# Kernel tuning notes

Hardware: AMD Instinct MI355X
Metric: run time of the kernel (lower is better)

Reference implementation:

```python
import jax, jax.numpy as jnp
import numpy as np

B, L, D, T = 32, 512, 1024, 256
MAX_MENTION_LEN = 10
NEG_INF = float('-inf')


def _static_bounds_and_keep():
    # Full (start, end) grid, flattened row-major like torch's .view(-1, 2)
    s = np.repeat(np.arange(L), L)
    e = np.tile(np.arange(L), L)
    bounds = np.stack([s, e], axis=-1)            # [L*L, 2]
    keep = (e - s) <= MAX_MENTION_LEN             # static per-position mask
    idx = np.nonzero(keep)[0]
    return jnp.asarray(bounds[keep], jnp.int32), jnp.asarray(idx, jnp.int32)


def setup_inputs() -> dict:
    key = jax.random.key(0)
    k0, k1, k2 = jax.random.split(key, 3)
    text_encodings = jax.random.normal(k0, (B, L, D), dtype=jnp.float32)
    mask_ctxt = jnp.ones((B, L), dtype=jnp.int32)
    # word -> wordpiece mapping: [start, end_exclusive); values kept in [1, L)
    tokens_mapping = jax.random.randint(k1, (B, T, 2), 1, L).astype(jnp.int32)
    W = jax.random.normal(k2, (D, 3), dtype=jnp.float32) * 0.02
    b = jnp.zeros((3,), dtype=jnp.float32)
    return {"text_encodings": text_encodings, "mask_ctxt": mask_ctxt,
            "tokens_mapping": tokens_mapping, "W": W, "b": b}


def reference(text_encodings, mask_ctxt, tokens_mapping, W, b):
    # per-token start / end / mention logits
    logits = jnp.einsum('bld,dk->blk', text_encodings, W) + b  # [B, L, 3]
    valid_tok = (mask_ctxt == 1)
    start_lp = jnp.where(valid_tok, logits[:, :, 0], NEG_INF)
    end_lp = jnp.where(valid_tok, logits[:, :, 1], NEG_INF)
    mention_lp = jnp.where(valid_tok, logits[:, :, 2], NEG_INF)

    # scores[b, s, e] = start[b, s] + end[b, e] + sum_{i=s..e} mention[b, i]
    scores = start_lp[:, :, None] + end_lp[:, None, :]          # [B, L, L]
    csum = jnp.cumsum(mention_lp, axis=1)                        # [B, L]
    csum_prev = jnp.concatenate(
        [jnp.zeros((csum.shape[0], 1), csum.dtype), csum[:, :-1]], axis=1)
    scores = scores + (csum[:, None, :] - csum_prev[:, :, None])

    # mention_sizes > 0  <=>  e >= s
    pos = jnp.arange(L)
    size_ok = pos[None, :, None] <= pos[None, None, :]           # [1, L, L]

    # token-boundary masks (scatter 1 at word starts / ends, zero col 0)
    bidx = jnp.arange(tokens_mapping.shape[0])[:, None]
    ts = jnp.zeros(mask_ctxt.shape, jnp.int32).at[bidx, tokens_mapping[:, :, 0]].set(1)
    ts = ts.at[:, 0].set(0)
    te = jnp.zeros(mask_ctxt.shape, jnp.int32).at[bidx, tokens_mapping[:, :, 1] - 1].set(1)
    te = te.at[:, 0].set(0)
    vse = ts[:, :, None] * te[:, None, :]                        # bmm outer product

    valid = size_ok & (mask_ctxt[:, :, None] > 0) & (vse > 0)
    scores = jnp.where(valid, scores, NEG_INF)

    scores_flat = scores.reshape(scores.shape[0], -1)            # [B, L*L]
    bounds_keep, keep_idx = _static_bounds_and_keep()
    out_scores = scores_flat[:, keep_idx]                        # [B, K]
    out_bounds = jnp.broadcast_to(bounds_keep[None],
                                  (scores.shape[0],) + bounds_keep.shape)
    return out_scores, out_bounds
```

## Files before the change

### kernel.cpp

```cpp
#include <hip/hip_runtime.h>
#include <math.h>

#define BB 32
#define LL 512
#define DD 1024
#define TT 256
#define NK 136393
#define NK_LIN 131273
#define S_LIN 502
#define NEG_BIG  -3.0e38f
#define NEG_MASK -1.0e30f

typedef float f4v __attribute__((ext_vector_type(4)));
typedef float f2v __attribute__((ext_vector_type(2)));

__global__ __launch_bounds__(256) void logits_kernel(
    const float* __restrict__ text, const float* __restrict__ W,
    const float* __restrict__ bias, const int* __restrict__ mask,
    const int* __restrict__ tmap,
    float* __restrict__ slp, float* __restrict__ elp, float* __restrict__ mlp,
    int* __restrict__ fs, int* __restrict__ fe)
{
    __shared__ int tsl[LL];
    __shared__ int tel[LL];
    const int wid  = threadIdx.x >> 6;
    const int lane = threadIdx.x & 63;
    const int row  = blockIdx.x * 4 + wid;
    const int b    = blockIdx.x;
    const int t    = threadIdx.x;

    if (b < BB) {
        tsl[t] = 0; tsl[t + 256] = 0;
        tel[t] = 0; tel[t + 256] = 0;
        __syncthreads();
        int s0 = tmap[((size_t)b * TT + t) * 2 + 0];
        int e0 = tmap[((size_t)b * TT + t) * 2 + 1] - 1;
        s0 = min(max(s0, 0), LL - 1);
        e0 = min(max(e0, 0), LL - 1);
        tsl[s0] = 1;
        tel[e0] = 1;
        __syncthreads();
    }

    const f4v* t4 = (const f4v*)(text + (size_t)row * DD);
    const f4v* w4 = (const f4v*)W;
    float a0 = 0.f, a1 = 0.f, a2 = 0.f;
#pragma unroll
    for (int j = 0; j < 4; ++j) {
        const int fi = lane + j * 64;
        f4v v  = __builtin_nontemporal_load(&t4[fi]);
        f4v w0 = w4[fi * 3 + 0];
        f4v w1 = w4[fi * 3 + 1];
        f4v w2 = w4[fi * 3 + 2];
        a0 += v.x * w0.x;  a1 += v.x * w0.y;  a2 += v.x * w0.z;
        a0 += v.y * w0.w;  a1 += v.y * w1.x;  a2 += v.y * w1.y;
        a0 += v.z * w1.z;  a1 += v.z * w1.w;  a2 += v.z * w2.x;
        a0 += v.w * w2.y;  a1 += v.w * w2.z;  a2 += v.w * w2.w;
    }
#pragma unroll
    for (int off = 32; off; off >>= 1) {
        a0 += __shfl_down(a0, off);
        a1 += __shfl_down(a1, off);
        a2 += __shfl_down(a2, off);
    }
    if (lane == 0) {
        const int m = mask[row];
        slp[row] = (m == 1) ? a0 + bias[0] : NEG_MASK;
        elp[row] = (m == 1) ? a1 + bias[1] : NEG_MASK;
        mlp[row] = (m == 1) ? a2 + bias[2] : NEG_MASK;
    }

    if (b < BB) {
        const int i0 = b * LL + t, i1 = i0 + 256;
        fs[i0] = (t != 0 && mask[i0] == 1 && tsl[t]) ? 1 : 0;
        fs[i1] = (mask[i1] == 1 && tsl[t + 256]) ? 1 : 0;
        fe[i0] = (t != 0 && tel[t]) ? 1 : 0;
        fe[i1] = tel[t + 256] ? 1 : 0;
    }
}

__global__ __launch_bounds__(256) void out_kernel(
    const float* __restrict__ slp, const float* __restrict__ elp,
    const float* __restrict__ mlp,
    const int* __restrict__ fs, const int* __restrict__ fe,
    float* __restrict__ out)
{
    const int s = blockIdx.x;
    const int b = blockIdx.y;
    const int t = threadIdx.x;
    const int rowlen = min(LL, s + 11);
    const size_t obase = (size_t)b * NK +
        (s <= S_LIN ? s * (s + 21) / 2 : NK_LIN + (s - S_LIN) * LL);
    const int base = b * LL;
    const int   fss = fs[base + s];
    const float sv  = slp[base + s];
    f2v* bptr = (f2v*)(out + (size_t)BB * NK);

#pragma unroll
    for (int h = 0; h < 2; ++h) {
        const int e = t + h * 256;
        if (e < rowlen) {
            float score = NEG_BIG;
            if (e >= s && fss && fe[base + e]) {
                float w = 0.f;
                for (int l = s; l <= e; ++l) w += mlp[base + l];
                score = (sv + elp[base + e]) + w;
            }
            __builtin_nontemporal_store(score, &out[obase + e]);
            f2v bv; bv.x = (float)s; bv.y = (float)e;
            __builtin_nontemporal_store(bv, &bptr[obase + e]);
        }
    }
}

extern "C" void kernel_launch(void* const* d_in, const int* in_sizes, int n_in,
                              void* d_out, int out_size, void* d_ws, size_t ws_size,
                              hipStream_t stream) {
    const float* text = (const float*)d_in[0];
    const int*   mask = (const int*)d_in[1];
    const int*   tmap = (const int*)d_in[2];
    const float* W    = (const float*)d_in[3];
    const float* bias = (const float*)d_in[4];
    float* out = (float*)d_out;

    float* slp = (float*)d_ws;
    float* elp = slp + (size_t)BB * LL;
    float* mlp = elp + (size_t)BB * LL;
    int*   fs  = (int*)(mlp + (size_t)BB * LL);
    int*   fe  = fs + (size_t)BB * LL;

    logits_kernel<<<BB * LL / 4, 256, 0, stream>>>(text, W, bias, mask, tmap,
                                                   slp, elp, mlp, fs, fe);
    dim3 g2(LL, BB);
    out_kernel<<<g2, 256, 0, stream>>>(slp, elp, mlp, fs, fe, out);
}
```

Measured before the change: 32.34 us.

## Fuse logits and output kernels into one block-per-row-range kernel

Merges the logits projection and the span-score writer into one kernel. Each block handles one batch and one of 16 row ranges, computing logits for its rows plus a 10-row halo into shared memory and then writing scores and bounds. The ranges come from a fixed split table chosen to balance output sizes, and the block-to-batch mapping groups each batch's blocks onto one XCD. This removes a launch and the workspace round trip, at the cost of recomputing halo rows and having only 512 blocks to hide latency.

```diff
diff --git a/kernel.cpp b/kernel.cpp
--- a/kernel.cpp
+++ b/kernel.cpp
@@ -10,105 +10,107 @@
 #define S_LIN 502
 #define NEG_BIG  -3.0e38f
 #define NEG_MASK -1.0e30f
+#define NRANGE 16
+#define MAXROWS 64
 
 typedef float f4v __attribute__((ext_vector_type(4)));
 typedef float f2v __attribute__((ext_vector_type(2)));
 
-__global__ __launch_bounds__(256) void logits_kernel(
+__device__ __constant__ int d_splits[NRANGE + 1] =
+    {0, 51, 97, 138, 177, 212, 246, 277, 308, 336, 364, 391, 417, 441, 466, 489, 512};
+
+__device__ __forceinline__ int off_s(int s) {
+    return (s <= S_LIN) ? s * (s + 21) / 2 : NK_LIN + (s - S_LIN) * LL;
+}
+
+__global__ __launch_bounds__(512, 4) void fused_kernel(
     const float* __restrict__ text, const float* __restrict__ W,
     const float* __restrict__ bias, const int* __restrict__ mask,
-    const int* __restrict__ tmap,
-    float* __restrict__ slp, float* __restrict__ elp, float* __restrict__ mlp,
-    int* __restrict__ fs, int* __restrict__ fe)
+    const int* __restrict__ tmap, float* __restrict__ out)
 {
-    __shared__ int tsl[LL];
-    __shared__ int tel[LL];
-    const int wid  = threadIdx.x >> 6;
-    const int lane = threadIdx.x & 63;
-    const int row  = blockIdx.x * 4 + wid;
-    const int b    = blockIdx.x;
-    const int t    = threadIdx.x;
+    __shared__ float sl[MAXROWS], el[MAXROWS], ml[MAXROWS];
+    __shared__ unsigned char tsl[LL], tel[LL];
 
-    if (b < BB) {
-        tsl[t] = 0; tsl[t + 256] = 0;
-        tel[t] = 0; tel[t + 256] = 0;
-        __syncthreads();
-        int s0 = tmap[((size_t)b * TT + t) * 2 + 0];
-        int e0 = tmap[((size_t)b * TT + t) * 2 + 1] - 1;
+    const int p    = blockIdx.x;
+    const int xcd  = p & 7, slot = p >> 3;
+    const int bb   = xcd * 4 + (slot >> 4);
+    const int ri   = slot & 15;
+    const int a    = d_splits[ri], bnd = d_splits[ri + 1];
+    const int rows_end = min(LL, bnd + 10);
+    const int nrows    = rows_end - a;
+
+    const int t = threadIdx.x;
+    const int wid = t >> 6, lane = t & 63;
+
+    tsl[t] = 0; tel[t] = 0;
+    __syncthreads();
+    if (t < TT) {
+        int s0 = tmap[((size_t)bb * TT + t) * 2 + 0];
+        int e0 = tmap[((size_t)bb * TT + t) * 2 + 1] - 1;
         s0 = min(max(s0, 0), LL - 1);
         e0 = min(max(e0, 0), LL - 1);
         tsl[s0] = 1;
         tel[e0] = 1;
-        __syncthreads();
     }
 
-    const f4v* t4 = (const f4v*)(text + (size_t)row * DD);
-    const f4v* w4 = (const f4v*)W;
-    float a0 = 0.f, a1 = 0.f, a2 = 0.f;
+    f4v wreg[12];
 #pragma unroll
     for (int j = 0; j < 4; ++j) {
         const int fi = lane + j * 64;
-        f4v v  = __builtin_nontemporal_load(&t4[fi]);
-        f4v w0 = w4[fi * 3 + 0];
-        f4v w1 = w4[fi * 3 + 1];
-        f4v w2 = w4[fi * 3 + 2];
-        a0 += v.x * w0.x;  a1 += v.x * w0.y;  a2 += v.x * w0.z;
-        a0 += v.y * w0.w;  a1 += v.y * w1.x;  a2 += v.y * w1.y;
-        a0 += v.z * w1.z;  a1 += v.z * w1.w;  a2 += v.z * w2.x;
-        a0 += v.w * w2.y;  a1 += v.w * w2.z;  a2 += v.w * w2.w;
+        wreg[j * 3 + 0] = ((const f4v*)W)[fi * 3 + 0];
+        wreg[j * 3 + 1] = ((const f4v*)W)[fi * 3 + 1];
+        wreg[j * 3 + 2] = ((const f4v*)W)[fi * 3 + 2];
     }
+    const float b0 = bias[0], b1 = bias[1], b2 = bias[2];
+
+    for (int r = wid; r < nrows; r += 8) {
+        const int row = bb * LL + a + r;
+        const f4v* t4 = (const f4v*)(text + (size_t)row * DD);
+        float a0 = 0.f, a1 = 0.f, a2 = 0.f;
 #pragma unroll
-    for (int off = 32; off; off >>= 1) {
-        a0 += __shfl_down(a0, off);
-        a1 += __shfl_down(a1, off);
-        a2 += __shfl_down(a2, off);
+        for (int j = 0; j < 4; ++j) {
+            f4v v  = __builtin_nontemporal_load(&t4[lane + j * 64]);
+            f4v w0 = wreg[j * 3], w1 = wreg[j * 3 + 1], w2 = wreg[j * 3 + 2];
+            a0 += v.x * w0.x;  a1 += v.x * w0.y;  a2 += v.x * w0.z;
+            a0 += v.y * w0.w;  a1 += v.y * w1.x;  a2 += v.y * w1.y;
+            a0 += v.z * w1.z;  a1 += v.z * w1.w;  a2 += v.z * w2.x;
+            a0 += v.w * w2.y;  a1 += v.w * w2.z;  a2 += v.w * w2.w;
+        }
+#pragma unroll
+        for (int o = 32; o; o >>= 1) {
+            a0 += __shfl_down(a0, o);
+            a1 += __shfl_down(a1, o);
+            a2 += __shfl_down(a2, o);
+        }
+        if (lane == 0) {
+            const int m = mask[row];
+            sl[r] = (m == 1) ? a0 + b0 : NEG_MASK;
+            el[r] = (m == 1) ? a1 + b1 : NEG_MASK;
+            ml[r] = (m == 1) ? a2 + b2 : NEG_MASK;
+        }
     }
-    if (lane == 0) {
-        const int m = mask[row];
-        slp[row] = (m == 1) ? a0 + bias[0] : NEG_MASK;
-        elp[row] = (m == 1) ? a1 + bias[1] : NEG_MASK;
-        mlp[row] = (m == 1) ? a2 + bias[2] : NEG_MASK;
-    }
+    __syncthreads();
 
-    if (b < BB) {
-        const int i0 = b * LL + t, i1 = i0 + 256;
-        fs[i0] = (t != 0 && mask[i0] == 1 && tsl[t]) ? 1 : 0;
-        fs[i1] = (mask[i1] == 1 && tsl[t + 256]) ? 1 : 0;
-        fe[i0] = (t != 0 && tel[t]) ? 1 : 0;
-        fe[i1] = tel[t + 256] ? 1 : 0;
-    }
-}
-
-__global__ __launch_bounds__(256) void out_kernel(
-    const float* __restrict__ slp, const float* __restrict__ elp,
-    const float* __restrict__ mlp,
-    const int* __restrict__ fs, const int* __restrict__ fe,
-    float* __restrict__ out)
-{
-    const int s = blockIdx.x;
-    const int b = blockIdx.y;
-    const int t = threadIdx.x;
-    const int rowlen = min(LL, s + 11);
-    const size_t obase = (size_t)b * NK +
-        (s <= S_LIN ? s * (s + 21) / 2 : NK_LIN + (s - S_LIN) * LL);
-    const int base = b * LL;
-    const int   fss = fs[base + s];
-    const float sv  = slp[base + s];
     f2v* bptr = (f2v*)(out + (size_t)BB * NK);
-
-#pragma unroll
-    for (int h = 0; h < 2; ++h) {
-        const int e = t + h * 256;
-        if (e < rowlen) {
-            float score = NEG_BIG;
-            if (e >= s && fss && fe[base + e]) {
-                float w = 0.f;
-                for (int l = s; l <= e; ++l) w += mlp[base + l];
-                score = (sv + elp[base + e]) + w;
+    for (int r = wid; r < bnd - a; r += 8) {
+        const int s = a + r;
+        const int fss = (s != 0) && tsl[s] && (mask[bb * LL + s] == 1);
+        const float sv = sl[r];
+        const int rowlen = min(LL, s + 11);
+        const size_t obase = (size_t)bb * NK + off_s(s);
+        for (int c = 0; c * 64 < rowlen; ++c) {
+            const int e = c * 64 + lane;
+            if (e < rowlen) {
+                float score = NEG_BIG;
+                if (e >= s && fss && e != 0 && tel[e]) {
+                    float w = 0.f;
+                    for (int l = r; l <= e - a; ++l) w += ml[l];
+                    score = sv + el[e - a] + w;
+                }
+                __builtin_nontemporal_store(score, &out[obase + e]);
+                f2v bv; bv.x = (float)s; bv.y = (float)e;
+                __builtin_nontemporal_store(bv, &bptr[obase + e]);
             }
-            __builtin_nontemporal_store(score, &out[obase + e]);
-            f2v bv; bv.x = (float)s; bv.y = (float)e;
-            __builtin_nontemporal_store(bv, &bptr[obase + e]);
         }
     }
 }
@@ -123,14 +125,5 @@
     const float* bias = (const float*)d_in[4];
     float* out = (float*)d_out;
 
-    float* slp = (float*)d_ws;
-    float* elp = slp + (size_t)BB * LL;
-    float* mlp = elp + (size_t)BB * LL;
-    int*   fs  = (int*)(mlp + (size_t)BB * LL);
-    int*   fe  = fs + (size_t)BB * LL;
-
-    logits_kernel<<<BB * LL / 4, 256, 0, stream>>>(text, W, bias, mask, tmap,
-                                                   slp, elp, mlp, fs, fe);
-    dim3 g2(LL, BB);
-    out_kernel<<<g2, 256, 0, stream>>>(slp, elp, mlp, fs, fe, out);
+    fused_kernel<<<BB * NRANGE, 512, 0, stream>>>(text, W, bias, mask, tmap, out);
 }
```

After: 40.03 us. +23.8%, slower.
